# Performance work log

Measured on AMD Instinct MI355X. Metric: run time of the kernel, lower is better.

Reference implementation:

```python
import jax, jax.numpy as jnp
import numpy as np

N = 100000   # nodes
E = 3200000  # edges (avg degree 32)
G = 64       # graphs in batch
H = 64       # hidden channels
EPS = 1e-5   # BatchNorm eps


def setup_inputs() -> dict:
    key = jax.random.key(0)
    ks = jax.random.split(key, 32)
    rn = lambda k, s: jax.random.normal(k, s, jnp.float32) * 0.1
    inp = {
        "x": jax.random.normal(ks[0], (N, 3), jnp.float32),
        "edge_index": jax.random.randint(ks[1], (2, E), 0, N),
        "batch": jnp.sort(jax.random.randint(ks[2], (N,), 0, G)),
    }
    dims = [(3, H), (H, H), (H, H)]
    for i, (di, do) in enumerate(dims):
        inp[f"W{i}"] = rn(ks[3 + i], (di, do))
        inp[f"b{i}"] = jnp.zeros((do,), jnp.float32)
        inp[f"g{i}"] = jnp.ones((do,), jnp.float32)
        inp[f"beta{i}"] = jnp.zeros((do,), jnp.float32)
    for j, p in enumerate(["p", "a", "t"]):
        out = 2 if p == "t" else 1
        inp[p + "W1"] = rn(ks[8 + 2 * j], (H, H // 2))
        inp[p + "b1"] = jnp.zeros((H // 2,), jnp.float32)
        inp[p + "W2"] = rn(ks[9 + 2 * j], (H // 2, out))
        inp[p + "b2"] = jnp.zeros((out,), jnp.float32)
    return inp


def _forward(x, edge_index, batch, params):
    (W0, b0, g0, beta0, W1, b1, g1, beta1, W2, b2, g2, beta2,
     pW1, pb1, pW2, pb2, aW1, ab1, aW2, ab2, tW1, tb1, tW2, tb2) = params
    src, dst = edge_index[0], edge_index[1]
    # GCN normalization with self-loops: deg = in-degree + 1
    deg = jax.ops.segment_sum(jnp.ones((E,), x.dtype), dst, num_segments=N) + 1.0
    dis = jax.lax.rsqrt(deg)  # deg^{-1/2}

    def gcn(h_in, W, b):
        h = h_in @ W  # [N, H]
        msg = h[src] * (dis[src] * dis[dst])[:, None]  # [E, H] gather
        out = jax.ops.segment_sum(msg, dst, num_segments=N)  # scatter-add
        out = out + h * (dis * dis)[:, None]  # self-loop term
        return out + b

    def bn_relu(h, g, be):
        m = jnp.mean(h, axis=0)
        v = jnp.var(h, axis=0)  # biased, as torch BN training mode
        return jax.nn.relu(g * (h - m) * jax.lax.rsqrt(v + EPS) + be)

    for W, b, g, be in [(W0, b0, g0, beta0), (W1, b1, g1, beta1), (W2, b2, g2, beta2)]:
        x = bn_relu(gcn(x, W, b), g, be)

    # global_mean_pool over graphs
    counts = jax.ops.segment_sum(jnp.ones((N,), x.dtype), batch, num_segments=G)
    pooled = jax.ops.segment_sum(x, batch, num_segments=G) / jnp.maximum(counts, 1.0)[:, None]

    def head(Wa, ba, Wb, bb):
        return jax.nn.relu(pooled @ Wa + ba) @ Wb + bb

    power = head(pW1, pb1, pW2, pb2)   # [G, 1]
    area = head(aW1, ab1, aW2, ab2)    # [G, 1]
    timing = head(tW1, tb1, tW2, tb2)  # [G, 2] = (tns, wns)
    return jnp.concatenate([power, area, timing], axis=1)  # [G, 4]


def reference(x, edge_index, batch, W0, b0, g0, beta0, W1, b1, g1, beta1,
              W2, b2, g2, beta2, pW1, pb1, pW2, pb2, aW1, ab1, aW2, ab2,
              tW1, tb1, tW2, tb2):
    params = (W0, b0, g0, beta0, W1, b1, g1, beta1, W2, b2, g2, beta2,
              pW1, pb1, pW2, pb2, aW1, ab1, aW2, ab2, tW1, tb1, tW2, tb2)
    return _forward(x, edge_index, batch, params)
```

## Files before the change

kernel.cpp:

```cpp
#include <hip/hip_runtime.h>
#include <hip/hip_fp16.h>

#define EPSBN 1e-5f
#define SH 7
#define CHUNK 16384
#define SCANB 256

__global__ void k_fill(float* __restrict__ p, float v, int n) {
    int i = blockIdx.x * blockDim.x + threadIdx.x;
    if (i < n) p[i] = v;
}

__launch_bounds__(1024)
__global__ void k_hist(const int* __restrict__ dst, int* __restrict__ hist,
                       int E, int C, int NB) {
    __shared__ int h[1024];
    const int tid = threadIdx.x, c = blockIdx.x;
    for (int i = tid; i < NB; i += 1024) h[i] = 0;
    __syncthreads();
    const int e0 = c * CHUNK, e1 = min(e0 + CHUNK, E);
    for (int e = e0 + tid; e < e1; e += 1024) atomicAdd(&h[dst[e] >> SH], 1);
    __syncthreads();
    for (int b = tid; b < NB; b += 1024) hist[b * C + c] = h[b];
}

__launch_bounds__(256)
__global__ void k_scanA(const int* __restrict__ hist, int* __restrict__ bsum, int M) {
    __shared__ int part[256];
    const int b = blockIdx.x, t = threadIdx.x;
    const int seg = (M + SCANB - 1) / SCANB;
    const int lo = b * seg, hi = min(lo + seg, M);
    int s = 0;
    for (int i = lo + t; i < hi; i += 256) s += hist[i];
    part[t] = s;
    __syncthreads();
    for (int d = 128; d > 0; d >>= 1) {
        if (t < d) part[t] += part[t + d];
        __syncthreads();
    }
    if (t == 0) bsum[b] = part[0];
}

__launch_bounds__(256)
__global__ void k_scanB(int* __restrict__ bsum) {
    __shared__ int sh[256];
    const int t = threadIdx.x;
    sh[t] = bsum[t];
    __syncthreads();
    for (int d = 1; d < 256; d <<= 1) {
        int v = (t >= d) ? sh[t - d] : 0;
        __syncthreads();
        sh[t] += v;
        __syncthreads();
    }
    bsum[t] = (t == 0) ? 0 : sh[t - 1];
}

__launch_bounds__(256)
__global__ void k_scanC(int* __restrict__ hist, const int* __restrict__ bsum,
                        int* __restrict__ off, int M, int E, int N) {
    __shared__ int part[256];
    const int b = blockIdx.x, t = threadIdx.x;
    const int seg = (M + SCANB - 1) / SCANB;
    const int lo = b * seg, hi = min(lo + seg, M);
    const int per = (seg + 255) >> 8;
    const int tl = lo + t * per, th = min(tl + per, hi);
    int s = 0;
    for (int i = tl; i < th; ++i) s += hist[i];
    part[t] = s;
    __syncthreads();
    for (int d = 1; d < 256; d <<= 1) {
        int v = (t >= d) ? part[t - d] : 0;
        __syncthreads();
        part[t] += v;
        __syncthreads();
    }
    int run = bsum[b] + ((t == 0) ? 0 : part[t - 1]);
    for (int i = tl; i < th; ++i) {
        int v = hist[i];
        hist[i] = run;
        run += v;
    }
    if (b == 0 && t == 0) off[N] = E;
}

__launch_bounds__(1024)
__global__ void k_sort(const int* __restrict__ src, const int* __restrict__ dst,
                       const int* __restrict__ hist, int* __restrict__ spk,
                       int E, int C, int NB) {
    __shared__ int cur[1024];
    const int tid = threadIdx.x, c = blockIdx.x;
    for (int b = tid; b < NB; b += 1024) cur[b] = hist[b * C + c];
    __syncthreads();
    const int e0 = c * CHUNK, e1 = min(e0 + CHUNK, E);
    for (int e = e0 + tid; e < e1; e += 1024) {
        const int d = dst[e];
        const int pos = atomicAdd(&cur[d >> SH], 1);
        spk[pos] = ((d & 127) << 18) | src[e];
    }
}

__launch_bounds__(256)
__global__ void k_csr(const int* __restrict__ spk, const int* __restrict__ hist,
                      int* __restrict__ off, float* __restrict__ dis,
                      int* __restrict__ eda, int E, int C, int NB, int N) {
    __shared__ int cnt_l[128], scn[128];
    const int tid = threadIdx.x, b = blockIdx.x;
    const int node0 = b << SH;
    const int nloc = min(128, N - node0);
    const int ebeg = hist[b * C];
    const int eend = (b + 1 < NB) ? hist[(b + 1) * C] : E;
    if (tid < 128) cnt_l[tid] = 0;
    __syncthreads();
    for (int e = ebeg + tid; e < eend; e += 256) {
        atomicAdd(&cnt_l[spk[e] >> 18], 1);
    }
    __syncthreads();
    if (tid < 128) scn[tid] = cnt_l[tid];
    __syncthreads();
    for (int d = 1; d < 128; d <<= 1) {
        int v = 0;
        if (tid < 128 && tid >= d) v = scn[tid - d];
        __syncthreads();
        if (tid < 128) scn[tid] += v;
        __syncthreads();
    }
    if (tid < nloc) {
        const int excl = scn[tid] - cnt_l[tid];
        off[node0 + tid] = ebeg + excl;
        dis[node0 + tid] = rsqrtf((float)cnt_l[tid] + 1.0f);
    }
    __syncthreads();
    if (tid < 128) cnt_l[tid] = scn[tid] - cnt_l[tid];
    __syncthreads();
    for (int e = ebeg + tid; e < eend; e += 256) {
        const int p = spk[e];
        const int r = atomicAdd(&cnt_l[p >> 18], 1);
        eda[ebeg + r] = p & 0x3FFFF;
    }
}

__global__ void k_prex(const float* __restrict__ x0, const float* __restrict__ dis,
                       float4* __restrict__ x0s4, int N) {
    int i = blockIdx.x * blockDim.x + threadIdx.x;
    if (i >= N) return;
    const float d = dis[i];
    x0s4[i] = make_float4(d * x0[3 * i], d * x0[3 * i + 1], d * x0[3 * i + 2], 0.f);
}

__launch_bounds__(256)
__global__ void k_gather3(const int* __restrict__ off, const int* __restrict__ eda,
                          const float* __restrict__ dis, const float4* __restrict__ x0s4,
                          float4* __restrict__ z4, int N) {
    const int lane = threadIdx.x & 63, wv = threadIdx.x >> 6;
    const int nw = gridDim.x * 4;
    for (int w = blockIdx.x * 4 + wv; w < N; w += nw) {
        const int e0 = off[w], e1 = off[w + 1];
        float a0 = 0.f, a1 = 0.f, a2 = 0.f;
        for (int e = e0 + lane; e < e1; e += 64) {
            float4 v = x0s4[eda[e]];
            a0 += v.x;
            a1 += v.y;
            a2 += v.z;
        }
        for (int d = 32; d; d >>= 1) {
            a0 += __shfl_xor(a0, d);
            a1 += __shfl_xor(a1, d);
            a2 += __shfl_xor(a2, d);
        }
        if (lane == 0) {
            const float4 sv = x0s4[w];
            const float dw = dis[w];
            z4[w] = make_float4(dw * (a0 + sv.x), dw * (a1 + sv.y), dw * (a2 + sv.z), 0.f);
        }
    }
}

__launch_bounds__(256)
__global__ void k_lin0(const float4* __restrict__ z4, const float* __restrict__ W,
                       float* __restrict__ bufA, float* __restrict__ st, int N) {
    __shared__ float Ws[3 * 64];
    __shared__ float ls[256], lq[256];
    const int tid = threadIdx.x;
    for (int i = tid; i < 192; i += 256) Ws[i] = W[i];
    __syncthreads();
    const int c = tid & 63, wv = tid >> 6;
    float s = 0.f, q = 0.f;
    for (int r = blockIdx.x * 4 + wv; r < N; r += gridDim.x * 4) {
        const float4 zr = z4[r];
        float acc = zr.x * Ws[c] + zr.y * Ws[64 + c] + zr.z * Ws[128 + c];
        bufA[(long)r * 64 + c] = acc;
        s += acc;
        q = fmaf(acc, acc, q);
    }
    ls[tid] = s;
    lq[tid] = q;
    __syncthreads();
    if (tid < 64) {
        s = ls[c] + ls[c + 64] + ls[c + 128] + ls[c + 192];
        q = lq[c] + lq[c + 64] + lq[c + 128] + lq[c + 192];
        unsafeAtomicAdd(&st[c], s);
        unsafeAtomicAdd(&st[64 + c], q);
    }
}

__launch_bounds__(256)
__global__ void k_linear(const float* __restrict__ X, const float* __restrict__ W,
                         const float* __restrict__ st, const float* __restrict__ g,
                         const float* __restrict__ be, const float* __restrict__ dis,
                         __half* __restrict__ hp, int N) {
    __shared__ float Ws[64 * 64];
    __shared__ float Xs[32 * 64];
    __shared__ float scs[64], shs[64];
    const int tid = threadIdx.x;
    if (tid < 64) {
        const float inv = 1.0f / (float)N;
        const float m = st[tid] * inv;
        const float v = st[64 + tid] * inv - m * m;
        const float sc = g[tid] * rsqrtf(v + EPSBN);
        scs[tid] = sc;
        shs[tid] = fmaf(-m, sc, be[tid]);
    }
    for (int i = tid; i < 64 * 64; i += 256) Ws[i] = W[i];
    __syncthreads();
    const int r0 = blockIdx.x * 32;
    for (int i = tid; i < 32 * 64; i += 256) {
        const int r = i >> 6, c = i & 63;
        const int row = r0 + r;
        float val = (row < N) ? X[(long)row * 64 + c] : 0.f;
        Xs[i] = fmaxf(fmaf(val, scs[c], shs[c]), 0.f);
    }
    __syncthreads();
    const int c = tid & 63, wv = tid >> 6;
    for (int rr = 0; rr < 8; ++rr) {
        const int r = wv * 8 + rr;
        const int row = r0 + r;
        if (row >= N) break;
        float acc = 0.f;
#pragma unroll
        for (int k = 0; k < 64; ++k) acc = fmaf(Xs[r * 64 + k], Ws[k * 64 + c], acc);
        hp[(long)row * 64 + c] = __float2half(acc * dis[row]);
    }
}

__launch_bounds__(256)
__global__ void k_gather(const int* __restrict__ off, const int* __restrict__ eda,
                         const float* __restrict__ dis, const __half* __restrict__ hp,
                         float* __restrict__ agg, float* __restrict__ st, int N) {
    __shared__ int els[4][64];
    __shared__ float ls[256], ls2[256];
    const int lane = threadIdx.x & 63;
    const int wv = threadIdx.x >> 6;
    const int nwaves = gridDim.x * 4;
    float s = 0.f, s2 = 0.f;
    for (int w = blockIdx.x * 4 + wv; w < N; w += nwaves) {
        const int e0 = off[w], e1 = off[w + 1];
        float acc0 = __half2float(hp[(long)w * 64 + lane]);
        float acc1 = 0.f, acc2 = 0.f, acc3 = 0.f;
        for (int eb = e0; eb < e1; eb += 64) {
            const int mm = min(64, e1 - eb);
            if (eb + lane < e1) els[wv][lane] = eda[eb + lane];
            int j = 0;
            for (; j + 8 <= mm; j += 8) {
                const int s0 = els[wv][j + 0], s1 = els[wv][j + 1];
                const int s2i = els[wv][j + 2], s3 = els[wv][j + 3];
                const int s4 = els[wv][j + 4], s5 = els[wv][j + 5];
                const int s6 = els[wv][j + 6], s7 = els[wv][j + 7];
                const float v0 = __half2float(hp[(long)s0 * 64 + lane]);
                const float v1 = __half2float(hp[(long)s1 * 64 + lane]);
                const float v2 = __half2float(hp[(long)s2i * 64 + lane]);
                const float v3 = __half2float(hp[(long)s3 * 64 + lane]);
                const float v4 = __half2float(hp[(long)s4 * 64 + lane]);
                const float v5 = __half2float(hp[(long)s5 * 64 + lane]);
                const float v6 = __half2float(hp[(long)s6 * 64 + lane]);
                const float v7 = __half2float(hp[(long)s7 * 64 + lane]);
                acc0 += v0 + v4;
                acc1 += v1 + v5;
                acc2 += v2 + v6;
                acc3 += v3 + v7;
            }
            for (; j < mm; ++j) acc0 += __half2float(hp[(long)els[wv][j] * 64 + lane]);
        }
        const float out = dis[w] * ((acc0 + acc1) + (acc2 + acc3));
        agg[(long)w * 64 + lane] = out;
        s += out;
        s2 = fmaf(out, out, s2);
    }
    ls[threadIdx.x] = s;
    ls2[threadIdx.x] = s2;
    __syncthreads();
    if (threadIdx.x < 64) {
        s = ls[lane] + ls[lane + 64] + ls[lane + 128] + ls[lane + 192];
        s2 = ls2[lane] + ls2[lane + 64] + ls2[lane + 128] + ls2[lane + 192];
        unsafeAtomicAdd(&st[lane], s);
        unsafeAtomicAdd(&st[64 + lane], s2);
    }
}

__launch_bounds__(256)
__global__ void k_pool(const float* __restrict__ x, const int* __restrict__ batch,
                       const float* __restrict__ st, const float* __restrict__ g,
                       const float* __restrict__ be, float* __restrict__ poolsum,
                       float* __restrict__ counts, int N, int npw) {
    const int wid = (blockIdx.x * blockDim.x + threadIdx.x) >> 6;
    const int lane = threadIdx.x & 63;
    const int n0 = wid * npw;
    if (n0 >= N) return;
    const float inv = 1.0f / (float)N;
    const float m = st[lane] * inv;
    const float v = st[64 + lane] * inv - m * m;
    const float sc = g[lane] * rsqrtf(v + EPSBN);
    const float sh = fmaf(-m, sc, be[lane]);
    const int n1 = min(n0 + npw, N);
    float acc = 0.f, cnt = 0.f;
    int gr = batch[n0];
    for (int n = n0; n < n1; ++n) {
        int gn = batch[n];
        if (gn != gr) {
            unsafeAtomicAdd(&poolsum[(long)gr * 64 + lane], acc);
            if (lane == 0) unsafeAtomicAdd(&counts[gr], cnt);
            acc = 0.f;
            cnt = 0.f;
            gr = gn;
        }
        acc += fmaxf(fmaf(x[(long)n * 64 + lane], sc, sh), 0.f);
        cnt += 1.f;
    }
    unsafeAtomicAdd(&poolsum[(long)gr * 64 + lane], acc);
    if (lane == 0) unsafeAtomicAdd(&counts[gr], cnt);
}

__launch_bounds__(256)
__global__ void k_heads(const float* __restrict__ poolsum, const float* __restrict__ counts,
                        const float* pW1, const float* pb1, const float* pW2, const float* pb2,
                        const float* aW1, const float* ab1, const float* aW2, const float* ab2,
                        const float* tW1, const float* tb1, const float* tW2, const float* tb2,
                        float* __restrict__ out, int G) {
    __shared__ float P[64 * 64];
    __shared__ float Hd[64 * 32];
    const int tid = threadIdx.x;
    for (int i = tid; i < G * 64; i += 256) {
        int g = i >> 6;
        P[i] = poolsum[i] / fmaxf(counts[g], 1.f);
    }
    __syncthreads();
    for (int j = 0; j < 3; ++j) {
        const float* W1 = (j == 0) ? pW1 : (j == 1) ? aW1 : tW1;
        const float* b1 = (j == 0) ? pb1 : (j == 1) ? ab1 : tb1;
        const float* W2 = (j == 0) ? pW2 : (j == 1) ? aW2 : tW2;
        const float* b2 = (j == 0) ? pb2 : (j == 1) ? ab2 : tb2;
        for (int i = tid; i < G * 32; i += 256) {
            int g = i >> 5, k = i & 31;
            float a = b1[k];
#pragma unroll
            for (int c = 0; c < 64; ++c) a = fmaf(P[g * 64 + c], W1[c * 32 + k], a);
            Hd[i] = fmaxf(a, 0.f);
        }
        __syncthreads();
        const int ow = (j == 2) ? 2 : 1;
        const int off = (j == 2) ? 2 : j;
        for (int i = tid; i < G * ow; i += 256) {
            int g = i / ow, o = i - g * ow;
            float a = b2[o];
#pragma unroll
            for (int k = 0; k < 32; ++k) a = fmaf(Hd[g * 32 + k], W2[k * ow + o], a);
            out[g * 4 + off + o] = a;
        }
        __syncthreads();
    }
}

extern "C" void kernel_launch(void* const* d_in, const int* in_sizes, int n_in,
                              void* d_out, int out_size, void* d_ws, size_t ws_size,
                              hipStream_t stream) {
    const int N = in_sizes[2];
    const int E = in_sizes[1] / 2;
    const int G = out_size / 4;

    const float* x0 = (const float*)d_in[0];
    const int* ei = (const int*)d_in[1];
    const int* src = ei;
    const int* dst = ei + E;
    const int* batch = (const int*)d_in[2];

    const float* W[3] = {(const float*)d_in[3], (const float*)d_in[7], (const float*)d_in[11]};
    const float* gam[3] = {(const float*)d_in[5], (const float*)d_in[9], (const float*)d_in[13]};
    const float* bet[3] = {(const float*)d_in[6], (const float*)d_in[10], (const float*)d_in[14]};

    const float* pW1 = (const float*)d_in[15];
    const float* pb1 = (const float*)d_in[16];
    const float* pW2 = (const float*)d_in[17];
    const float* pb2 = (const float*)d_in[18];
    const float* aW1 = (const float*)d_in[19];
    const float* ab1 = (const float*)d_in[20];
    const float* aW2 = (const float*)d_in[21];
    const float* ab2 = (const float*)d_in[22];
    const float* tW1 = (const float*)d_in[23];
    const float* tb1 = (const float*)d_in[24];
    const float* tW2 = (const float*)d_in[25];
    const float* tb2 = (const float*)d_in[26];

    const int C = (E + CHUNK - 1) / CHUNK;
    const int NB = (N + 127) >> SH;
    const int M = NB * C;

    auto align = [](size_t x) { return (x + 255) & ~(size_t)255; };
    char* w = (char*)d_ws;
    float* dis = (float*)w;      w += align((size_t)N * 4);
    float* bufA = (float*)w;     w += align((size_t)N * 64 * 4);
    __half* hp = (__half*)w;     w += align((size_t)N * 64 * 2);
    float* st = (float*)w;       w += align(3 * 128 * 4);
    float* poolsum = (float*)w;  w += align((size_t)G * 64 * 4);
    float* counts = (float*)w;   w += align((size_t)G * 4);
    int* off = (int*)w;          w += align((size_t)(N + 1) * 4);
    int* hist = (int*)w;         w += align((size_t)M * 4);
    int* bsum = (int*)w;         w += align((size_t)SCANB * 4);
    int* spk = (int*)w;          w += align((size_t)E * 4);
    int* eda = (int*)w;          w += align((size_t)E * 4);
    float4* x0s4 = (float4*)w;   w += align((size_t)N * 16);
    float4* z4 = (float4*)w;     w += align((size_t)N * 16);
    (void)ws_size;

    const int nbN = (N + 255) / 256;
    const int nb_lin = (N + 31) / 32;
    const int nb_ga = 2048;

    k_hist<<<C, 1024, 0, stream>>>(dst, hist, E, C, NB);
    k_scanA<<<SCANB, 256, 0, stream>>>(hist, bsum, M);
    k_scanB<<<1, 256, 0, stream>>>(bsum);
    k_scanC<<<SCANB, 256, 0, stream>>>(hist, bsum, off, M, E, N);
    k_sort<<<C, 1024, 0, stream>>>(src, dst, hist, spk, E, C, NB);
    k_csr<<<NB, 256, 0, stream>>>(spk, hist, off, dis, eda, E, C, NB, N);
    k_fill<<<2, 256, 0, stream>>>(st, 0.f, 3 * 128);

    k_prex<<<nbN, 256, 0, stream>>>(x0, dis, x0s4, N);
    k_gather3<<<512, 256, 0, stream>>>(off, eda, dis, x0s4, z4, N);
    k_lin0<<<1024, 256, 0, stream>>>(z4, W[0], bufA, st, N);

    for (int l = 1; l < 3; ++l) {
        k_linear<<<nb_lin, 256, 0, stream>>>(bufA, W[l], st + (l - 1) * 128,
                                             gam[l - 1], bet[l - 1], dis, hp, N);
        k_gather<<<nb_ga, 256, 0, stream>>>(off, eda, dis, hp, bufA, st + l * 128, N);
    }

    k_fill<<<(G * 64 + 255) / 256, 256, 0, stream>>>(poolsum, 0.f, G * 64);
    k_fill<<<1, 64, 0, stream>>>(counts, 0.f, G);
    const int npw = 32;
    const int nwaves = (N + npw - 1) / npw;
    const int nb_pool = (nwaves * 64 + 255) / 256;
    k_pool<<<nb_pool, 256, 0, stream>>>(bufA, batch, st + 256, gam[2], bet[2],
                                        poolsum, counts, N, npw);

    k_heads<<<1, 256, 0, stream>>>(poolsum, counts, pW1, pb1, pW2, pb2,
                                   aW1, ab1, aW2, ab2, tW1, tb1, tW2, tb2,
                                   (float*)d_out, G);
}
```

Baseline: 506.0 us.

## Fuse fills, prescale and layer-0 kernels; gather two nodes per wave

The buffer-zeroing fills move into k_scanB, and the x0 prescale moves into k_csr. The layer-0 gather is fused with the 3x64 linear and its BN statistics into one kernel, k_gl0, which removes the z4 intermediate. The hidden-layer gather now handles two nodes per wave (p and p+P) with interleaved loads to expose more memory-level parallelism, but uses a 4-wide unroll per node instead of 8. Together these cut about five kernel launches and one round trip of intermediate data, at the cost of more complex gather control flow and possible load imbalance between the paired nodes.

After: 472.3 us. 6.7% less time.

```diff
diff --git a/kernel.cpp b/kernel.cpp
--- a/kernel.cpp
+++ b/kernel.cpp
@@ -5,11 +5,6 @@
 #define SH 7
 #define CHUNK 16384
 #define SCANB 256
-
-__global__ void k_fill(float* __restrict__ p, float v, int n) {
-    int i = blockIdx.x * blockDim.x + threadIdx.x;
-    if (i < n) p[i] = v;
-}
 
 __launch_bounds__(1024)
 __global__ void k_hist(const int* __restrict__ dst, int* __restrict__ hist,
@@ -42,7 +37,8 @@
 }
 
 __launch_bounds__(256)
-__global__ void k_scanB(int* __restrict__ bsum) {
+__global__ void k_scanB(int* __restrict__ bsum, float* __restrict__ st,
+                        float* __restrict__ poolsum, float* __restrict__ counts, int G) {
     __shared__ int sh[256];
     const int t = threadIdx.x;
     sh[t] = bsum[t];
@@ -54,6 +50,9 @@
         __syncthreads();
     }
     bsum[t] = (t == 0) ? 0 : sh[t - 1];
+    for (int i = t; i < 3 * 128; i += 256) st[i] = 0.f;
+    for (int i = t; i < G * 64; i += 256) poolsum[i] = 0.f;
+    for (int i = t; i < G; i += 256) counts[i] = 0.f;
 }
 
 __launch_bounds__(256)
@@ -102,7 +101,8 @@
 
 __launch_bounds__(256)
 __global__ void k_csr(const int* __restrict__ spk, const int* __restrict__ hist,
-                      int* __restrict__ off, float* __restrict__ dis,
+                      const float* __restrict__ x0, int* __restrict__ off,
+                      float* __restrict__ dis, float4* __restrict__ x0s4,
                       int* __restrict__ eda, int E, int C, int NB, int N) {
     __shared__ int cnt_l[128], scn[128];
     const int tid = threadIdx.x, b = blockIdx.x;
@@ -127,8 +127,11 @@
     }
     if (tid < nloc) {
         const int excl = scn[tid] - cnt_l[tid];
-        off[node0 + tid] = ebeg + excl;
-        dis[node0 + tid] = rsqrtf((float)cnt_l[tid] + 1.0f);
+        const int i = node0 + tid;
+        const float d = rsqrtf((float)cnt_l[tid] + 1.0f);
+        off[i] = ebeg + excl;
+        dis[i] = d;
+        x0s4[i] = make_float4(d * x0[3 * i], d * x0[3 * i + 1], d * x0[3 * i + 2], 0.f);
     }
     __syncthreads();
     if (tid < 128) cnt_l[tid] = scn[tid] - cnt_l[tid];
@@ -140,20 +143,19 @@
     }
 }
 
-__global__ void k_prex(const float* __restrict__ x0, const float* __restrict__ dis,
-                       float4* __restrict__ x0s4, int N) {
-    int i = blockIdx.x * blockDim.x + threadIdx.x;
-    if (i >= N) return;
-    const float d = dis[i];
-    x0s4[i] = make_float4(d * x0[3 * i], d * x0[3 * i + 1], d * x0[3 * i + 2], 0.f);
-}
-
-__launch_bounds__(256)
-__global__ void k_gather3(const int* __restrict__ off, const int* __restrict__ eda,
-                          const float* __restrict__ dis, const float4* __restrict__ x0s4,
-                          float4* __restrict__ z4, int N) {
-    const int lane = threadIdx.x & 63, wv = threadIdx.x >> 6;
+__launch_bounds__(256)
+__global__ void k_gl0(const int* __restrict__ off, const int* __restrict__ eda,
+                      const float* __restrict__ dis, const float4* __restrict__ x0s4,
+                      const float* __restrict__ W0, float* __restrict__ bufA,
+                      float* __restrict__ st, int N) {
+    __shared__ float Ws[192];
+    __shared__ float ls[256], lq[256];
+    const int tid = threadIdx.x;
+    const int lane = tid & 63, wv = tid >> 6;
+    for (int i = tid; i < 192; i += 256) Ws[i] = W0[i];
+    __syncthreads();
     const int nw = gridDim.x * 4;
+    float s = 0.f, q = 0.f;
     for (int w = blockIdx.x * 4 + wv; w < N; w += nw) {
         const int e0 = off[w], e1 = off[w + 1];
         float a0 = 0.f, a1 = 0.f, a2 = 0.f;
@@ -163,44 +165,28 @@
             a1 += v.y;
             a2 += v.z;
         }
+#pragma unroll
         for (int d = 32; d; d >>= 1) {
             a0 += __shfl_xor(a0, d);
             a1 += __shfl_xor(a1, d);
             a2 += __shfl_xor(a2, d);
         }
-        if (lane == 0) {
-            const float4 sv = x0s4[w];
-            const float dw = dis[w];
-            z4[w] = make_float4(dw * (a0 + sv.x), dw * (a1 + sv.y), dw * (a2 + sv.z), 0.f);
-        }
-    }
-}
-
-__launch_bounds__(256)
-__global__ void k_lin0(const float4* __restrict__ z4, const float* __restrict__ W,
-                       float* __restrict__ bufA, float* __restrict__ st, int N) {
-    __shared__ float Ws[3 * 64];
-    __shared__ float ls[256], lq[256];
-    const int tid = threadIdx.x;
-    for (int i = tid; i < 192; i += 256) Ws[i] = W[i];
-    __syncthreads();
-    const int c = tid & 63, wv = tid >> 6;
-    float s = 0.f, q = 0.f;
-    for (int r = blockIdx.x * 4 + wv; r < N; r += gridDim.x * 4) {
-        const float4 zr = z4[r];
-        float acc = zr.x * Ws[c] + zr.y * Ws[64 + c] + zr.z * Ws[128 + c];
-        bufA[(long)r * 64 + c] = acc;
-        s += acc;
-        q = fmaf(acc, acc, q);
+        const float4 sv = x0s4[w];
+        const float dw = dis[w];
+        const float z0 = dw * (a0 + sv.x), z1 = dw * (a1 + sv.y), z2 = dw * (a2 + sv.z);
+        const float val = z0 * Ws[lane] + z1 * Ws[64 + lane] + z2 * Ws[128 + lane];
+        bufA[(long)w * 64 + lane] = val;
+        s += val;
+        q = fmaf(val, val, q);
     }
     ls[tid] = s;
     lq[tid] = q;
     __syncthreads();
     if (tid < 64) {
-        s = ls[c] + ls[c + 64] + ls[c + 128] + ls[c + 192];
-        q = lq[c] + lq[c + 64] + lq[c + 128] + lq[c + 192];
-        unsafeAtomicAdd(&st[c], s);
-        unsafeAtomicAdd(&st[64 + c], q);
+        s = ls[lane] + ls[lane + 64] + ls[lane + 128] + ls[lane + 192];
+        q = lq[lane] + lq[lane + 64] + lq[lane + 128] + lq[lane + 192];
+        unsafeAtomicAdd(&st[lane], s);
+        unsafeAtomicAdd(&st[64 + lane], q);
     }
 }
 
@@ -247,44 +233,94 @@
 __global__ void k_gather(const int* __restrict__ off, const int* __restrict__ eda,
                          const float* __restrict__ dis, const __half* __restrict__ hp,
                          float* __restrict__ agg, float* __restrict__ st, int N) {
-    __shared__ int els[4][64];
+    __shared__ int els[4][2][64];
     __shared__ float ls[256], ls2[256];
     const int lane = threadIdx.x & 63;
     const int wv = threadIdx.x >> 6;
     const int nwaves = gridDim.x * 4;
+    const int P = (N + 1) >> 1;
     float s = 0.f, s2 = 0.f;
-    for (int w = blockIdx.x * 4 + wv; w < N; w += nwaves) {
-        const int e0 = off[w], e1 = off[w + 1];
-        float acc0 = __half2float(hp[(long)w * 64 + lane]);
-        float acc1 = 0.f, acc2 = 0.f, acc3 = 0.f;
-        for (int eb = e0; eb < e1; eb += 64) {
-            const int mm = min(64, e1 - eb);
-            if (eb + lane < e1) els[wv][lane] = eda[eb + lane];
+    for (int p = blockIdx.x * 4 + wv; p < P; p += nwaves) {
+        const int wA = p, wB = p + P;
+        const bool hasB = (wB < N);
+        const int a0o = off[wA];
+        const int nA = off[wA + 1] - a0o;
+        const int b0o = hasB ? off[wB] : 0;
+        const int nB = hasB ? off[wB + 1] - b0o : 0;
+        float accA0 = __half2float(hp[(long)wA * 64 + lane]);
+        float accA1 = 0.f, accA2 = 0.f, accA3 = 0.f;
+        float accB0 = hasB ? __half2float(hp[(long)wB * 64 + lane]) : 0.f;
+        float accB1 = 0.f, accB2 = 0.f, accB3 = 0.f;
+        const int nmax = nA > nB ? nA : nB;
+        for (int base = 0; base < nmax; base += 64) {
+            if (base + lane < nA) els[wv][0][lane] = eda[a0o + base + lane];
+            if (base + lane < nB) els[wv][1][lane] = eda[b0o + base + lane];
+            int mA = nA - base;
+            mA = mA < 0 ? 0 : (mA > 64 ? 64 : mA);
+            int mB = nB - base;
+            mB = mB < 0 ? 0 : (mB > 64 ? 64 : mB);
+            const int mc = mA < mB ? mA : mB;
             int j = 0;
-            for (; j + 8 <= mm; j += 8) {
-                const int s0 = els[wv][j + 0], s1 = els[wv][j + 1];
-                const int s2i = els[wv][j + 2], s3 = els[wv][j + 3];
-                const int s4 = els[wv][j + 4], s5 = els[wv][j + 5];
-                const int s6 = els[wv][j + 6], s7 = els[wv][j + 7];
-                const float v0 = __half2float(hp[(long)s0 * 64 + lane]);
-                const float v1 = __half2float(hp[(long)s1 * 64 + lane]);
-                const float v2 = __half2float(hp[(long)s2i * 64 + lane]);
-                const float v3 = __half2float(hp[(long)s3 * 64 + lane]);
-                const float v4 = __half2float(hp[(long)s4 * 64 + lane]);
-                const float v5 = __half2float(hp[(long)s5 * 64 + lane]);
-                const float v6 = __half2float(hp[(long)s6 * 64 + lane]);
-                const float v7 = __half2float(hp[(long)s7 * 64 + lane]);
-                acc0 += v0 + v4;
-                acc1 += v1 + v5;
-                acc2 += v2 + v6;
-                acc3 += v3 + v7;
+            for (; j + 4 <= mc; j += 4) {
+                const int sa0 = els[wv][0][j + 0], sa1 = els[wv][0][j + 1];
+                const int sa2 = els[wv][0][j + 2], sa3 = els[wv][0][j + 3];
+                const int sb0 = els[wv][1][j + 0], sb1 = els[wv][1][j + 1];
+                const int sb2 = els[wv][1][j + 2], sb3 = els[wv][1][j + 3];
+                const float va0 = __half2float(hp[(long)sa0 * 64 + lane]);
+                const float va1 = __half2float(hp[(long)sa1 * 64 + lane]);
+                const float va2 = __half2float(hp[(long)sa2 * 64 + lane]);
+                const float va3 = __half2float(hp[(long)sa3 * 64 + lane]);
+                const float vb0 = __half2float(hp[(long)sb0 * 64 + lane]);
+                const float vb1 = __half2float(hp[(long)sb1 * 64 + lane]);
+                const float vb2 = __half2float(hp[(long)sb2 * 64 + lane]);
+                const float vb3 = __half2float(hp[(long)sb3 * 64 + lane]);
+                accA0 += va0;
+                accA1 += va1;
+                accA2 += va2;
+                accA3 += va3;
+                accB0 += vb0;
+                accB1 += vb1;
+                accB2 += vb2;
+                accB3 += vb3;
             }
-            for (; j < mm; ++j) acc0 += __half2float(hp[(long)els[wv][j] * 64 + lane]);
-        }
-        const float out = dis[w] * ((acc0 + acc1) + (acc2 + acc3));
-        agg[(long)w * 64 + lane] = out;
-        s += out;
-        s2 = fmaf(out, out, s2);
+            int jA = j, jB = j;
+            for (; jA + 4 <= mA; jA += 4) {
+                const int sa0 = els[wv][0][jA + 0], sa1 = els[wv][0][jA + 1];
+                const int sa2 = els[wv][0][jA + 2], sa3 = els[wv][0][jA + 3];
+                const float va0 = __half2float(hp[(long)sa0 * 64 + lane]);
+                const float va1 = __half2float(hp[(long)sa1 * 64 + lane]);
+                const float va2 = __half2float(hp[(long)sa2 * 64 + lane]);
+                const float va3 = __half2float(hp[(long)sa3 * 64 + lane]);
+                accA0 += va0;
+                accA1 += va1;
+                accA2 += va2;
+                accA3 += va3;
+            }
+            for (; jA < mA; ++jA) accA0 += __half2float(hp[(long)els[wv][0][jA] * 64 + lane]);
+            for (; jB + 4 <= mB; jB += 4) {
+                const int sb0 = els[wv][1][jB + 0], sb1 = els[wv][1][jB + 1];
+                const int sb2 = els[wv][1][jB + 2], sb3 = els[wv][1][jB + 3];
+                const float vb0 = __half2float(hp[(long)sb0 * 64 + lane]);
+                const float vb1 = __half2float(hp[(long)sb1 * 64 + lane]);
+                const float vb2 = __half2float(hp[(long)sb2 * 64 + lane]);
+                const float vb3 = __half2float(hp[(long)sb3 * 64 + lane]);
+                accB0 += vb0;
+                accB1 += vb1;
+                accB2 += vb2;
+                accB3 += vb3;
+            }
+            for (; jB < mB; ++jB) accB0 += __half2float(hp[(long)els[wv][1][jB] * 64 + lane]);
+        }
+        const float outA = dis[wA] * ((accA0 + accA1) + (accA2 + accA3));
+        agg[(long)wA * 64 + lane] = outA;
+        s += outA;
+        s2 = fmaf(outA, outA, s2);
+        if (hasB) {
+            const float outB = dis[wB] * ((accB0 + accB1) + (accB2 + accB3));
+            agg[(long)wB * 64 + lane] = outB;
+            s += outB;
+            s2 = fmaf(outB, outB, s2);
+        }
     }
     ls[threadIdx.x] = s;
     ls2[threadIdx.x] = s2;
@@ -418,24 +454,19 @@
     int* spk = (int*)w;          w += align((size_t)E * 4);
     int* eda = (int*)w;          w += align((size_t)E * 4);
     float4* x0s4 = (float4*)w;   w += align((size_t)N * 16);
-    float4* z4 = (float4*)w;     w += align((size_t)N * 16);
     (void)ws_size;
 
-    const int nbN = (N + 255) / 256;
     const int nb_lin = (N + 31) / 32;
     const int nb_ga = 2048;
 
     k_hist<<<C, 1024, 0, stream>>>(dst, hist, E, C, NB);
     k_scanA<<<SCANB, 256, 0, stream>>>(hist, bsum, M);
-    k_scanB<<<1, 256, 0, stream>>>(bsum);
+    k_scanB<<<1, 256, 0, stream>>>(bsum, st, poolsum, counts, G);
     k_scanC<<<SCANB, 256, 0, stream>>>(hist, bsum, off, M, E, N);
     k_sort<<<C, 1024, 0, stream>>>(src, dst, hist, spk, E, C, NB);
-    k_csr<<<NB, 256, 0, stream>>>(spk, hist, off, dis, eda, E, C, NB, N);
-    k_fill<<<2, 256, 0, stream>>>(st, 0.f, 3 * 128);
-
-    k_prex<<<nbN, 256, 0, stream>>>(x0, dis, x0s4, N);
-    k_gather3<<<512, 256, 0, stream>>>(off, eda, dis, x0s4, z4, N);
-    k_lin0<<<1024, 256, 0, stream>>>(z4, W[0], bufA, st, N);
+    k_csr<<<NB, 256, 0, stream>>>(spk, hist, x0, off, dis, x0s4, eda, E, C, NB, N);
+
+    k_gl0<<<2048, 256, 0, stream>>>(off, eda, dis, x0s4, W[0], bufA, st, N);
 
     for (int l = 1; l < 3; ++l) {
         k_linear<<<nb_lin, 256, 0, stream>>>(bufA, W[l], st + (l - 1) * 128,
@@ -443,8 +474,6 @@
         k_gather<<<nb_ga, 256, 0, stream>>>(off, eda, dis, hp, bufA, st + l * 128, N);
     }
 
-    k_fill<<<(G * 64 + 255) / 256, 256, 0, stream>>>(poolsum, 0.f, G * 64);
-    k_fill<<<1, 64, 0, stream>>>(counts, 0.f, G);
     const int npw = 32;
     const int nwaves = (N + npw - 1) / npw;
     const int nb_pool = (nwaves * 64 + 255) / 256;
```
